# Optimization experiments

Measured on AMD Instinct MI355X. Metric: run time of the kernel, lower is better.

The kernel has to match this reference:

```python
import jax, jax.numpy as jnp
import numpy as np

B, H, D, RD = 32, 16, 256, 64          # batch, heads, head_dim, rotary_dim
NE, NI = 4096, 16384                   # n_embd, n_inner
SLOTS, KVL = 32768, 1024               # paged cache slots, per-batch kv length
EPS = 1e-5


def setup_inputs() -> dict:
    key = jax.random.key(0)
    ks = jax.random.split(key, 12)
    s = 0.02
    return {
        "hidden_states": jax.random.normal(ks[0], (B, 1, NE), jnp.float32),
        "key_cache": jax.random.normal(ks[1], (SLOTS, H, D), jnp.float32),
        "value_cache": jax.random.normal(ks[2], (SLOTS, H, D), jnp.float32),
        "ln_w": jnp.ones((NE,), jnp.float32),
        "ln_b": jnp.zeros((NE,), jnp.float32),
        "wq": jax.random.normal(ks[3], (NE, NE), jnp.float32) * s,
        "wk": jax.random.normal(ks[4], (NE, NE), jnp.float32) * s,
        "wv": jax.random.normal(ks[5], (NE, NE), jnp.float32) * s,
        "wo": jax.random.normal(ks[6], (NE, NE), jnp.float32) * s,
        "fc_in_w": jax.random.normal(ks[7], (NE, NI), jnp.float32) * s,
        "fc_in_b": jnp.zeros((NI,), jnp.float32),
        "fc_out_w": jax.random.normal(ks[8], (NI, NE), jnp.float32) * s,
        "fc_out_b": jnp.zeros((NE,), jnp.float32),
        "attention_mask": jnp.zeros((B, 1, 1, KVL), jnp.float32),
        "new_key_location": jnp.arange(B, dtype=jnp.int32),
        "new_value_location": jnp.arange(B, dtype=jnp.int32),
        "past_valid_key_decode_indices": jax.random.randint(ks[9], (B, KVL), 0, SLOTS, jnp.int32),
        "past_valid_value_decode_indices": jax.random.randint(ks[10], (B, KVL), 0, SLOTS, jnp.int32),
        "position_ids": jax.random.randint(ks[11], (B, 1), 0, KVL, jnp.int32),
    }


def _rope(x, position_ids):
    # GPT-J rotate-every-two rotary on first RD dims. x: [B, S, H, D]
    half = RD // 2
    inv_freq = 1.0 / (10000.0 ** (jnp.arange(0, RD, 2, dtype=jnp.float32) / RD))  # [half]
    ang = position_ids.astype(jnp.float32)[..., None] * inv_freq  # [B, S, half]
    sin = jnp.sin(ang)[:, :, None, :]  # [B, S, 1, half]
    cos = jnp.cos(ang)[:, :, None, :]
    xr, xp = x[..., :RD], x[..., RD:]
    x1, x2 = xr[..., 0::2], xr[..., 1::2]
    o1 = x1 * cos - x2 * sin
    o2 = x2 * cos + x1 * sin
    rot = jnp.stack([o1, o2], axis=-1).reshape(xr.shape)
    return jnp.concatenate([rot, xp], axis=-1)


def reference(hidden_states, key_cache, value_cache, ln_w, ln_b, wq, wk, wv, wo,
              fc_in_w, fc_in_b, fc_out_w, fc_out_b, attention_mask,
              new_key_location, new_value_location,
              past_valid_key_decode_indices, past_valid_value_decode_indices,
              position_ids):
    residual = hidden_states[:, -1:, :]                       # [B, 1, NE]
    mu = jnp.mean(hidden_states, axis=-1, keepdims=True)
    var = jnp.mean(jnp.square(hidden_states - mu), axis=-1, keepdims=True)
    h = (hidden_states - mu) * jax.lax.rsqrt(var + EPS) * ln_w + ln_b

    q = (h @ wq).reshape(B, 1, H, D)
    k = (h @ wk).reshape(B, 1, H, D)
    v = (h @ wv).reshape(B, 1, H, D)
    q = _rope(q, position_ids)
    k = _rope(k, position_ids)

    # paged KV update: scatter new token, gather valid slots per batch
    kc = key_cache.at[new_key_location].set(k[:, 0])          # [SLOTS, H, D]
    vc = value_cache.at[new_value_location].set(v[:, 0])
    K = kc[past_valid_key_decode_indices]                     # [B, KVL, H, D]
    V = vc[past_valid_value_decode_indices]                   # [B, KVL, H, D]

    scale = jnp.asarray(np.sqrt(D), jnp.float32)
    scores = jnp.einsum("bqhd,blhd->bhql", q, K) / scale + attention_mask
    p = jax.nn.softmax(scores, axis=-1)                       # [B, H, 1, KVL]
    ctx = jnp.einsum("bhql,blhd->bqhd", p, V).reshape(B, 1, NE)
    attn_out = ctx @ wo

    m = jax.nn.gelu(h[:, -1:, :] @ fc_in_w + fc_in_b, approximate=True)
    mlp_out = m @ fc_out_w + fc_out_b

    return attn_out + mlp_out + residual
```

## Files before the change

### kernel.cpp

```cpp
#include <hip/hip_runtime.h>
#include <math.h>

#define BB 32
#define HH 16
#define DD 256
#define RDIM 64
#define NEMB 4096
#define NINT 16384
#define NSLOTS 32768
#define KVLEN 1024
#define LNEPS 1e-5f
#define NCH 16
#define CH 64

__global__ __launch_bounds__(256) void ln_kernel(const float* __restrict__ x,
    const float* __restrict__ lw, const float* __restrict__ lb,
    float* __restrict__ hT)
{
    int b = blockIdx.x;
    int t = threadIdx.x;
    const float* row = x + (size_t)b * NEMB;
    float4 v[4];
    float sum = 0.f, sq = 0.f;
#pragma unroll
    for (int j = 0; j < 4; ++j) {
        v[j] = *(const float4*)(row + t * 4 + j * 1024);
        sum += v[j].x + v[j].y + v[j].z + v[j].w;
        sq += v[j].x * v[j].x + v[j].y * v[j].y + v[j].z * v[j].z + v[j].w * v[j].w;
    }
    __shared__ float s1[4], s2[4];
#pragma unroll
    for (int o = 32; o > 0; o >>= 1) {
        sum += __shfl_xor(sum, o, 64);
        sq += __shfl_xor(sq, o, 64);
    }
    int wave = t >> 6, lane = t & 63;
    if (lane == 0) { s1[wave] = sum; s2[wave] = sq; }
    __syncthreads();
    sum = s1[0] + s1[1] + s1[2] + s1[3];
    sq = s2[0] + s2[1] + s2[2] + s2[3];
    float mu = sum / NEMB;
    float var = sq / NEMB - mu * mu;
    float rstd = rsqrtf(var + LNEPS);
#pragma unroll
    for (int j = 0; j < 4; ++j) {
        int n = t * 4 + j * 1024;
        float4 wv = *(const float4*)(lw + n);
        float4 bv = *(const float4*)(lb + n);
        hT[(size_t)(n + 0) * BB + b] = (v[j].x - mu) * rstd * wv.x + bv.x;
        hT[(size_t)(n + 1) * BB + b] = (v[j].y - mu) * rstd * wv.y + bv.y;
        hT[(size_t)(n + 2) * BB + b] = (v[j].z - mu) * rstd * wv.z + bv.z;
        hT[(size_t)(n + 3) * BB + b] = (v[j].w - mu) * rstd * wv.w + bv.w;
    }
}

__device__ __forceinline__ void gemm_body(const float* __restrict__ AT,
    const float* __restrict__ W, float* __restrict__ P,
    int N, int kChunk, int x, int s)
{
    int n = (x * 256 + threadIdx.x) * 2;
    size_t k0 = (size_t)s * kChunk;
    float2 acc[32];
#pragma unroll
    for (int mi = 0; mi < 32; ++mi) acc[mi] = make_float2(0.f, 0.f);
    const float* w = W + k0 * N + n;
    const float* a = AT + k0 * 32;
#pragma unroll 4
    for (int kk = 0; kk < kChunk; ++kk) {
        float2 wv = *(const float2*)w;
#pragma unroll
        for (int mi = 0; mi < 32; ++mi) {
            float am = a[mi];
            acc[mi].x = fmaf(am, wv.x, acc[mi].x);
            acc[mi].y = fmaf(am, wv.y, acc[mi].y);
        }
        w += N;
        a += 32;
    }
    float* p = P + ((size_t)s * 32) * N + n;
#pragma unroll
    for (int mi = 0; mi < 32; ++mi)
        *(float2*)(p + (size_t)mi * N) = acc[mi];
}

__global__ __launch_bounds__(256) void gemm_qkv_kernel(const float* __restrict__ AT,
    const float* __restrict__ W0, const float* __restrict__ W1, const float* __restrict__ W2,
    float* __restrict__ P)
{
    const float* W = (blockIdx.z == 0) ? W0 : (blockIdx.z == 1) ? W1 : W2;
    float* Pz = P + (size_t)blockIdx.z * ((size_t)32 * 32 * NEMB);
    gemm_body(AT, W, Pz, NEMB, 128, blockIdx.x, blockIdx.y);
}

__global__ __launch_bounds__(256) void gemm_dual_kernel(
    const float* __restrict__ ctxT, const float* __restrict__ wo, float* __restrict__ P0,
    const float* __restrict__ hT, const float* __restrict__ fciw, float* __restrict__ P1)
{
    int id = blockIdx.x;
    if (id < 512) gemm_body(ctxT, wo, P0, NEMB, 64, id & 7, id >> 3);
    else { id -= 512; gemm_body(hT, fciw, P1, NINT, 256, id & 31, id >> 5); }
}

__global__ __launch_bounds__(256) void gemm_fcout_kernel(const float* __restrict__ AT,
    const float* __restrict__ W, float* __restrict__ P)
{
    gemm_body(AT, W, P, NEMB, 256, blockIdx.x, blockIdx.y);
}

__device__ inline float gelu_tanh(float x)
{
    float x3 = x * x * x;
    return 0.5f * x * (1.f + tanhf(0.7978845608028654f * (x + 0.044715f * x3)));
}

__global__ __launch_bounds__(256) void qkv_rr_kernel(const float* __restrict__ P,
    float* __restrict__ q, float* __restrict__ k, float* __restrict__ v,
    const int* __restrict__ pos)
{
    int w = blockIdx.z;
    int m = blockIdx.y;
    int n0 = (blockIdx.x * 256 + threadIdx.x) * 2;
    const float* p = P + (size_t)w * ((size_t)32 * 32 * NEMB) + (size_t)m * NEMB + n0;
    float sx = 0.f, sy = 0.f;
#pragma unroll 4
    for (int i = 0; i < 32; ++i) {
        float2 u = *(const float2*)p;
        sx += u.x; sy += u.y;
        p += (size_t)32 * NEMB;
    }
    int d = n0 & (DD - 1);
    if (w < 2 && d < RDIM) {
        int i = d >> 1;
        float fr = exp2f((float)i * (-13.287712379549449f / 32.f));
        float ang = (float)pos[m] * fr;
        float sn, cs;
        sincosf(ang, &sn, &cs);
        float x1 = sx, x2 = sy;
        sx = x1 * cs - x2 * sn;
        sy = x2 * cs + x1 * sn;
    }
    float* o = (w == 0) ? q : (w == 1) ? k : v;
    *(float2*)(o + (size_t)m * NEMB + n0) = make_float2(sx, sy);
}

__global__ __launch_bounds__(256) void reduce_dual_kernel(
    const float* __restrict__ P0, const float* __restrict__ P1,
    const float* __restrict__ fcib, float* __restrict__ attn_o, float* __restrict__ mT)
{
    int bx = blockIdx.x, m = blockIdx.y, t = threadIdx.x;
    if (bx < 16) {
        int n = bx * 256 + t;
        const float* p = P0 + (size_t)m * NEMB + n;
        float s = 0.f;
#pragma unroll 4
        for (int i = 0; i < 64; ++i) { s += *p; p += (size_t)32 * NEMB; }
        attn_o[(size_t)m * NEMB + n] = s;
    } else {
        int n = (bx - 16) * 256 + t;
        const float* p = P1 + (size_t)m * NINT + n;
        float s = 0.f;
#pragma unroll 4
        for (int i = 0; i < 16; ++i) { s += *p; p += (size_t)32 * NINT; }
        mT[(size_t)n * 32 + m] = gelu_tanh(s + fcib[n]);
    }
}

__global__ __launch_bounds__(256) void reduce_final_kernel(const float* __restrict__ P,
    const float* __restrict__ bias, const float* __restrict__ attn_o,
    const float* __restrict__ resid, float* __restrict__ out)
{
    int n = blockIdx.x * 256 + threadIdx.x;
    int m = blockIdx.y;
    const float* p = P + (size_t)m * NEMB + n;
    float s = 0.f;
#pragma unroll 4
    for (int i = 0; i < 64; ++i) { s += *p; p += (size_t)32 * NEMB; }
    out[(size_t)m * NEMB + n] = s + bias[n] + attn_o[(size_t)m * NEMB + n]
                              + resid[(size_t)m * NEMB + n];
}

__global__ __launch_bounds__(256) void attn_part_kernel(const float* __restrict__ q,
    const float* __restrict__ knew, const float* __restrict__ vnew,
    const float* __restrict__ kcache, const float* __restrict__ vcache,
    const int* __restrict__ kidx, const int* __restrict__ vidx,
    const int* __restrict__ nkl, const int* __restrict__ nvl,
    const float* __restrict__ mask,
    float* __restrict__ pm, float* __restrict__ pl, float* __restrict__ pctx)
{
    int b = blockIdx.x >> 4, h = blockIdx.x & 15, c = blockIdx.y;
    int t = threadIdx.x;
    __shared__ float qs[DD];
    __shared__ float sc[CH];
    __shared__ const float* kp[CH];
    __shared__ const float* vp[CH];
    __shared__ float cx[4][DD];

    qs[t] = q[(size_t)b * NEMB + (size_t)h * DD + t];
    if (t < CH) {
        int l = c * CH + t;
        int ks = kidx[b * KVLEN + l];
        int vs = vidx[b * KVLEN + l];
        const float* kbase = kcache + (size_t)ks * NEMB;
        const float* vbase = vcache + (size_t)vs * NEMB;
#pragma unroll
        for (int j = 0; j < BB; ++j) {
            if (nkl[j] == ks) kbase = knew + (size_t)j * NEMB;
            if (nvl[j] == vs) vbase = vnew + (size_t)j * NEMB;
        }
        kp[t] = kbase + (size_t)h * DD;
        vp[t] = vbase + (size_t)h * DD;
    }
    __syncthreads();

    int wave = t >> 6, lane = t & 63;
    float4 qf = *(const float4*)(qs + lane * 4);
#pragma unroll 4
    for (int l = wave; l < CH; l += 4) {
        const float4 kf = *(const float4*)(kp[l] + lane * 4);
        float d = fmaf(kf.x, qf.x, fmaf(kf.y, qf.y, fmaf(kf.z, qf.z, kf.w * qf.w)));
#pragma unroll
        for (int o = 32; o > 0; o >>= 1) d += __shfl_xor(d, o, 64);
        if (lane == 0) sc[l] = d * 0.0625f + mask[b * KVLEN + c * CH + l];
    }
    __syncthreads();

    float sv = sc[lane];
    float mx = sv;
#pragma unroll
    for (int o = 32; o > 0; o >>= 1) mx = fmaxf(mx, __shfl_xor(mx, o, 64));
    float e = expf(sv - mx);
    float sm = e;
#pragma unroll
    for (int o = 32; o > 0; o >>= 1) sm += __shfl_xor(sm, o, 64);
    if (t < CH) sc[t] = e;
    __syncthreads();

    float4 a4 = make_float4(0.f, 0.f, 0.f, 0.f);
#pragma unroll 4
    for (int l = wave; l < CH; l += 4) {
        float4 vf = *(const float4*)(vp[l] + lane * 4);
        float pw = sc[l];
        a4.x = fmaf(pw, vf.x, a4.x);
        a4.y = fmaf(pw, vf.y, a4.y);
        a4.z = fmaf(pw, vf.z, a4.z);
        a4.w = fmaf(pw, vf.w, a4.w);
    }
    *(float4*)(&cx[wave][lane * 4]) = a4;
    __syncthreads();

    int pi = blockIdx.x * NCH + c;
    pctx[(size_t)pi * DD + t] = cx[0][t] + cx[1][t] + cx[2][t] + cx[3][t];
    if (t == 0) { pm[pi] = mx; pl[pi] = sm; }
}

__global__ __launch_bounds__(256) void attn_comb_kernel(const float* __restrict__ pm,
    const float* __restrict__ pl, const float* __restrict__ pctx,
    float* __restrict__ ctxT)
{
    int bh = blockIdx.x;
    int b = bh >> 4, h = bh & 15;
    int t = threadIdx.x;
    float M = -INFINITY;
#pragma unroll
    for (int c = 0; c < NCH; ++c) M = fmaxf(M, pm[bh * NCH + c]);
    float L = 0.f, acc = 0.f;
#pragma unroll
    for (int c = 0; c < NCH; ++c) {
        float wv = expf(pm[bh * NCH + c] - M);
        L += pl[bh * NCH + c] * wv;
        acc += pctx[((size_t)bh * NCH + c) * DD + t] * wv;
    }
    ctxT[((size_t)h * DD + t) * BB + b] = acc / L;
}

extern "C" void kernel_launch(void* const* d_in, const int* in_sizes, int n_in,
                              void* d_out, int out_size, void* d_ws, size_t ws_size,
                              hipStream_t stream)
{
    (void)in_sizes; (void)n_in; (void)out_size; (void)ws_size;
    const float* hs      = (const float*)d_in[0];
    const float* kcache  = (const float*)d_in[1];
    const float* vcache  = (const float*)d_in[2];
    const float* ln_w    = (const float*)d_in[3];
    const float* ln_b    = (const float*)d_in[4];
    const float* wq      = (const float*)d_in[5];
    const float* wk      = (const float*)d_in[6];
    const float* wv      = (const float*)d_in[7];
    const float* wo      = (const float*)d_in[8];
    const float* fc_in_w = (const float*)d_in[9];
    const float* fc_in_b = (const float*)d_in[10];
    const float* fc_out_w= (const float*)d_in[11];
    const float* fc_out_b= (const float*)d_in[12];
    const float* mask    = (const float*)d_in[13];
    const int* nkl       = (const int*)d_in[14];
    const int* nvl       = (const int*)d_in[15];
    const int* kidx      = (const int*)d_in[16];
    const int* vidx      = (const int*)d_in[17];
    const int* pos       = (const int*)d_in[18];
    float* out = (float*)d_out;

    char* ws = (char*)d_ws;
    float* hT      = (float*)ws; ws += (size_t)NEMB * BB * 4;
    float* qb      = (float*)ws; ws += (size_t)BB * NEMB * 4;
    float* kb      = (float*)ws; ws += (size_t)BB * NEMB * 4;
    float* vb      = (float*)ws; ws += (size_t)BB * NEMB * 4;
    float* ctxT    = (float*)ws; ws += (size_t)NEMB * BB * 4;
    float* attn_o  = (float*)ws; ws += (size_t)BB * NEMB * 4;
    float* mT      = (float*)ws; ws += (size_t)NINT * BB * 4;
    float* pm      = (float*)ws; ws += (size_t)BB * HH * NCH * 4;
    float* pl      = (float*)ws; ws += (size_t)BB * HH * NCH * 4;
    float* pctx    = (float*)ws; ws += (size_t)BB * HH * NCH * DD * 4;
    float* Pq      = (float*)ws; ws += (size_t)3 * 32 * 32 * NEMB * 4;
    float* P0      = (float*)ws; ws += (size_t)64 * 32 * NEMB * 4;
    float* P1      = (float*)ws; ws += (size_t)16 * 32 * NINT * 4;
    float* P2      = (float*)ws;

    ln_kernel<<<BB, 256, 0, stream>>>(hs, ln_w, ln_b, hT);

    gemm_qkv_kernel<<<dim3(8, 32, 3), 256, 0, stream>>>(hT, wq, wk, wv, Pq);
    qkv_rr_kernel<<<dim3(8, 32, 3), 256, 0, stream>>>(Pq, qb, kb, vb, pos);

    attn_part_kernel<<<dim3(BB * HH, NCH), 256, 0, stream>>>(qb, kb, vb, kcache, vcache,
                                                             kidx, vidx, nkl, nvl, mask,
                                                             pm, pl, pctx);
    attn_comb_kernel<<<BB * HH, 256, 0, stream>>>(pm, pl, pctx, ctxT);

    gemm_dual_kernel<<<1024, 256, 0, stream>>>(ctxT, wo, P0, hT, fc_in_w, P1);
    reduce_dual_kernel<<<dim3(80, 32), 256, 0, stream>>>(P0, P1, fc_in_b, attn_o, mT);

    gemm_fcout_kernel<<<dim3(8, 64), 256, 0, stream>>>(mT, fc_out_w, P2);
    reduce_final_kernel<<<dim3(16, 32), 256, 0, stream>>>(P2, fc_out_b, attn_o, hs, out);
}
```

Baseline: 541.9 us.

## Reschedule kernels to overlap MLP branch with attention path in merged launches

The independent MLP branch is interleaved with the attention path by merging unrelated work into shared launches. The fc_in GEMM runs alongside the QKV GEMM, the fc_in reduction and GELU alongside the QKV reduce and RoPE, and the fc_out GEMM alongside the paged attention partials. The fc_out reduction runs next to the wo GEMM, leaving one final reduce that adds the attention output. This cuts the dependent launch count and fills idle CUs during the latency-bound attention and GEMM phases. It mixes heterogeneous blocks in one grid, which may imbalance scheduling or raise memory contention during attention.

```diff
diff --git a/kernel.cpp b/kernel.cpp
--- a/kernel.cpp
+++ b/kernel.cpp
@@ -83,28 +83,20 @@
         *(float2*)(p + (size_t)mi * N) = acc[mi];
 }
 
-__global__ __launch_bounds__(256) void gemm_qkv_kernel(const float* __restrict__ AT,
-    const float* __restrict__ W0, const float* __restrict__ W1, const float* __restrict__ W2,
-    float* __restrict__ P)
-{
-    const float* W = (blockIdx.z == 0) ? W0 : (blockIdx.z == 1) ? W1 : W2;
-    float* Pz = P + (size_t)blockIdx.z * ((size_t)32 * 32 * NEMB);
-    gemm_body(AT, W, Pz, NEMB, 128, blockIdx.x, blockIdx.y);
-}
-
-__global__ __launch_bounds__(256) void gemm_dual_kernel(
-    const float* __restrict__ ctxT, const float* __restrict__ wo, float* __restrict__ P0,
-    const float* __restrict__ hT, const float* __restrict__ fciw, float* __restrict__ P1)
+__global__ __launch_bounds__(256) void phase2_kernel(const float* __restrict__ hT,
+    const float* __restrict__ wq, const float* __restrict__ wk, const float* __restrict__ wv,
+    float* __restrict__ Pq, const float* __restrict__ fciw, float* __restrict__ P1)
 {
     int id = blockIdx.x;
-    if (id < 512) gemm_body(ctxT, wo, P0, NEMB, 64, id & 7, id >> 3);
-    else { id -= 512; gemm_body(hT, fciw, P1, NINT, 256, id & 31, id >> 5); }
-}
-
-__global__ __launch_bounds__(256) void gemm_fcout_kernel(const float* __restrict__ AT,
-    const float* __restrict__ W, float* __restrict__ P)
-{
-    gemm_body(AT, W, P, NEMB, 256, blockIdx.x, blockIdx.y);
+    if (id < 768) {
+        int w = id >> 8;
+        const float* W = (w == 0) ? wq : (w == 1) ? wk : wv;
+        float* Pz = Pq + (size_t)w * ((size_t)32 * 32 * NEMB);
+        gemm_body(hT, W, Pz, NEMB, 128, id & 7, (id >> 3) & 31);
+    } else {
+        id -= 768;
+        gemm_body(hT, fciw, P1, NINT, 256, id & 31, id >> 5);
+    }
 }
 
 __device__ inline float gelu_tanh(float x)
@@ -113,50 +105,41 @@
     return 0.5f * x * (1.f + tanhf(0.7978845608028654f * (x + 0.044715f * x3)));
 }
 
-__global__ __launch_bounds__(256) void qkv_rr_kernel(const float* __restrict__ P,
+__global__ __launch_bounds__(256) void phase3_kernel(const float* __restrict__ Pq,
     float* __restrict__ q, float* __restrict__ k, float* __restrict__ v,
-    const int* __restrict__ pos)
-{
-    int w = blockIdx.z;
-    int m = blockIdx.y;
-    int n0 = (blockIdx.x * 256 + threadIdx.x) * 2;
-    const float* p = P + (size_t)w * ((size_t)32 * 32 * NEMB) + (size_t)m * NEMB + n0;
-    float sx = 0.f, sy = 0.f;
-#pragma unroll 4
-    for (int i = 0; i < 32; ++i) {
-        float2 u = *(const float2*)p;
-        sx += u.x; sy += u.y;
-        p += (size_t)32 * NEMB;
-    }
-    int d = n0 & (DD - 1);
-    if (w < 2 && d < RDIM) {
-        int i = d >> 1;
-        float fr = exp2f((float)i * (-13.287712379549449f / 32.f));
-        float ang = (float)pos[m] * fr;
-        float sn, cs;
-        sincosf(ang, &sn, &cs);
-        float x1 = sx, x2 = sy;
-        sx = x1 * cs - x2 * sn;
-        sy = x2 * cs + x1 * sn;
-    }
-    float* o = (w == 0) ? q : (w == 1) ? k : v;
-    *(float2*)(o + (size_t)m * NEMB + n0) = make_float2(sx, sy);
-}
-
-__global__ __launch_bounds__(256) void reduce_dual_kernel(
-    const float* __restrict__ P0, const float* __restrict__ P1,
-    const float* __restrict__ fcib, float* __restrict__ attn_o, float* __restrict__ mT)
-{
-    int bx = blockIdx.x, m = blockIdx.y, t = threadIdx.x;
-    if (bx < 16) {
-        int n = bx * 256 + t;
-        const float* p = P0 + (size_t)m * NEMB + n;
-        float s = 0.f;
-#pragma unroll 4
-        for (int i = 0; i < 64; ++i) { s += *p; p += (size_t)32 * NEMB; }
-        attn_o[(size_t)m * NEMB + n] = s;
+    const int* __restrict__ pos,
+    const float* __restrict__ P1, const float* __restrict__ fcib, float* __restrict__ mT)
+{
+    int id = blockIdx.x, t = threadIdx.x;
+    if (id < 768) {
+        int w = id >> 8;
+        int m = (id >> 3) & 31;
+        int n0 = ((id & 7) * 256 + t) * 2;
+        const float* p = Pq + (size_t)w * ((size_t)32 * 32 * NEMB) + (size_t)m * NEMB + n0;
+        float sx = 0.f, sy = 0.f;
+#pragma unroll 4
+        for (int i = 0; i < 32; ++i) {
+            float2 u = *(const float2*)p;
+            sx += u.x; sy += u.y;
+            p += (size_t)32 * NEMB;
+        }
+        int d = n0 & (DD - 1);
+        if (w < 2 && d < RDIM) {
+            int i = d >> 1;
+            float fr = exp2f((float)i * (-13.287712379549449f / 32.f));
+            float ang = (float)pos[m] * fr;
+            float sn, cs;
+            sincosf(ang, &sn, &cs);
+            float x1 = sx, x2 = sy;
+            sx = x1 * cs - x2 * sn;
+            sy = x2 * cs + x1 * sn;
+        }
+        float* o = (w == 0) ? q : (w == 1) ? k : v;
+        *(float2*)(o + (size_t)m * NEMB + n0) = make_float2(sx, sy);
     } else {
-        int n = (bx - 16) * 256 + t;
+        int j = id - 768;
+        int m = j >> 6;
+        int n = (j & 63) * 256 + t;
         const float* p = P1 + (size_t)m * NINT + n;
         float s = 0.f;
 #pragma unroll 4
@@ -165,29 +148,23 @@
     }
 }
 
-__global__ __launch_bounds__(256) void reduce_final_kernel(const float* __restrict__ P,
-    const float* __restrict__ bias, const float* __restrict__ attn_o,
-    const float* __restrict__ resid, float* __restrict__ out)
-{
-    int n = blockIdx.x * 256 + threadIdx.x;
-    int m = blockIdx.y;
-    const float* p = P + (size_t)m * NEMB + n;
-    float s = 0.f;
-#pragma unroll 4
-    for (int i = 0; i < 64; ++i) { s += *p; p += (size_t)32 * NEMB; }
-    out[(size_t)m * NEMB + n] = s + bias[n] + attn_o[(size_t)m * NEMB + n]
-                              + resid[(size_t)m * NEMB + n];
-}
-
-__global__ __launch_bounds__(256) void attn_part_kernel(const float* __restrict__ q,
+__global__ __launch_bounds__(256) void phase4_kernel(const float* __restrict__ q,
     const float* __restrict__ knew, const float* __restrict__ vnew,
     const float* __restrict__ kcache, const float* __restrict__ vcache,
     const int* __restrict__ kidx, const int* __restrict__ vidx,
     const int* __restrict__ nkl, const int* __restrict__ nvl,
     const float* __restrict__ mask,
-    float* __restrict__ pm, float* __restrict__ pl, float* __restrict__ pctx)
-{
-    int b = blockIdx.x >> 4, h = blockIdx.x & 15, c = blockIdx.y;
+    float* __restrict__ pm, float* __restrict__ pl, float* __restrict__ pctx,
+    const float* __restrict__ mT, const float* __restrict__ fcow, float* __restrict__ P2)
+{
+    int id = blockIdx.x;
+    if (id >= 8192) {
+        int j = id - 8192;
+        gemm_body(mT, fcow, P2, NEMB, 256, j & 7, j >> 3);
+        return;
+    }
+    int bh = id >> 4, c = id & 15;
+    int b = bh >> 4, h = bh & 15;
     int t = threadIdx.x;
     __shared__ float qs[DD];
     __shared__ float sc[CH];
@@ -248,7 +225,7 @@
     *(float4*)(&cx[wave][lane * 4]) = a4;
     __syncthreads();
 
-    int pi = blockIdx.x * NCH + c;
+    int pi = bh * NCH + c;
     pctx[(size_t)pi * DD + t] = cx[0][t] + cx[1][t] + cx[2][t] + cx[3][t];
     if (t == 0) { pm[pi] = mx; pl[pi] = sm; }
 }
@@ -271,6 +248,38 @@
         acc += pctx[((size_t)bh * NCH + c) * DD + t] * wv;
     }
     ctxT[((size_t)h * DD + t) * BB + b] = acc / L;
+}
+
+__global__ __launch_bounds__(256) void phase6_kernel(const float* __restrict__ ctxT,
+    const float* __restrict__ wo, float* __restrict__ P0,
+    const float* __restrict__ P2, const float* __restrict__ fcob,
+    const float* __restrict__ resid, float* __restrict__ mlp_tmp)
+{
+    int id = blockIdx.x, t = threadIdx.x;
+    if (id < 512) {
+        gemm_body(ctxT, wo, P0, NEMB, 64, id & 7, id >> 3);
+    } else {
+        int j = id - 512;
+        int m = j >> 4;
+        int n = (j & 15) * 256 + t;
+        const float* p = P2 + (size_t)m * NEMB + n;
+        float s = 0.f;
+#pragma unroll 4
+        for (int i = 0; i < 64; ++i) { s += *p; p += (size_t)32 * NEMB; }
+        mlp_tmp[(size_t)m * NEMB + n] = s + fcob[n] + resid[(size_t)m * NEMB + n];
+    }
+}
+
+__global__ __launch_bounds__(256) void phase7_kernel(const float* __restrict__ P0,
+    const float* __restrict__ mlp_tmp, float* __restrict__ out)
+{
+    int n = blockIdx.x * 256 + threadIdx.x;
+    int m = blockIdx.y;
+    const float* p = P0 + (size_t)m * NEMB + n;
+    float s = 0.f;
+#pragma unroll 4
+    for (int i = 0; i < 64; ++i) { s += *p; p += (size_t)32 * NEMB; }
+    out[(size_t)m * NEMB + n] = s + mlp_tmp[(size_t)m * NEMB + n];
 }
 
 extern "C" void kernel_launch(void* const* d_in, const int* in_sizes, int n_in,
@@ -305,7 +314,7 @@
     float* kb      = (float*)ws; ws += (size_t)BB * NEMB * 4;
     float* vb      = (float*)ws; ws += (size_t)BB * NEMB * 4;
     float* ctxT    = (float*)ws; ws += (size_t)NEMB * BB * 4;
-    float* attn_o  = (float*)ws; ws += (size_t)BB * NEMB * 4;
+    float* mlp_tmp = (float*)ws; ws += (size_t)BB * NEMB * 4;
     float* mT      = (float*)ws; ws += (size_t)NINT * BB * 4;
     float* pm      = (float*)ws; ws += (size_t)BB * HH * NCH * 4;
     float* pl      = (float*)ws; ws += (size_t)BB * HH * NCH * 4;
@@ -317,17 +326,17 @@
 
     ln_kernel<<<BB, 256, 0, stream>>>(hs, ln_w, ln_b, hT);
 
-    gemm_qkv_kernel<<<dim3(8, 32, 3), 256, 0, stream>>>(hT, wq, wk, wv, Pq);
-    qkv_rr_kernel<<<dim3(8, 32, 3), 256, 0, stream>>>(Pq, qb, kb, vb, pos);
-
-    attn_part_kernel<<<dim3(BB * HH, NCH), 256, 0, stream>>>(qb, kb, vb, kcache, vcache,
-                                                             kidx, vidx, nkl, nvl, mask,
-                                                             pm, pl, pctx);
+    phase2_kernel<<<1280, 256, 0, stream>>>(hT, wq, wk, wv, Pq, fc_in_w, P1);
+
+    phase3_kernel<<<2816, 256, 0, stream>>>(Pq, qb, kb, vb, pos, P1, fc_in_b, mT);
+
+    phase4_kernel<<<8704, 256, 0, stream>>>(qb, kb, vb, kcache, vcache,
+                                            kidx, vidx, nkl, nvl, mask,
+                                            pm, pl, pctx, mT, fc_out_w, P2);
+
     attn_comb_kernel<<<BB * HH, 256, 0, stream>>>(pm, pl, pctx, ctxT);
 
-    gemm_dual_kernel<<<1024, 256, 0, stream>>>(ctxT, wo, P0, hT, fc_in_w, P1);
-    reduce_dual_kernel<<<dim3(80, 32), 256, 0, stream>>>(P0, P1, fc_in_b, attn_o, mT);
-
-    gemm_fcout_kernel<<<dim3(8, 64), 256, 0, stream>>>(mT, fc_out_w, P2);
-    reduce_final_kernel<<<dim3(16, 32), 256, 0, stream>>>(P2, fc_out_b, attn_o, hs, out);
-}
+    phase6_kernel<<<1024, 256, 0, stream>>>(ctxT, wo, P0, P2, fc_out_b, hs, mlp_tmp);
+
+    phase7_kernel<<<dim3(16, 32), 256, 0, stream>>>(P0, mlp_tmp, out);
+}
```

Measured after the change: 513.9 us. 5.2% less time.
